# Performance work log

Measured on AMD Instinct MI355X. Metric: run time of the kernel, lower is better.

The kernel has to match this reference:

```python
import jax, jax.numpy as jnp
import numpy as np

EMBED_DIM = 1024
NUM_HEADS = 16
HEAD_DIM = EMBED_DIM // NUM_HEADS
BATCH = 4
SEQ = 2048


def setup_inputs() -> dict:
    key = jax.random.key(0)
    k1, k2, k3 = jax.random.split(key, 3)
    scale = 0.02
    x = jax.random.normal(k1, (BATCH, SEQ, EMBED_DIM), dtype=jnp.float32)
    Wqkv = jax.random.normal(k2, (EMBED_DIM, 3 * EMBED_DIM), dtype=jnp.float32) * scale
    bqkv = jnp.zeros((3 * EMBED_DIM,), dtype=jnp.float32)
    Wout = jax.random.normal(k3, (EMBED_DIM, EMBED_DIM), dtype=jnp.float32) * scale
    bout = jnp.zeros((EMBED_DIM,), dtype=jnp.float32)
    # causal mask: 1 where attention is allowed (lower triangle), 0 elsewhere
    mask = jnp.tril(jnp.ones((SEQ, SEQ), dtype=jnp.int32))
    return {"x": x, "mask": mask, "Wqkv": Wqkv, "bqkv": bqkv, "Wout": Wout, "bout": bout}


def reference(x, mask, Wqkv, bqkv, Wout, bout):
    B, S, E = x.shape
    H, D = NUM_HEADS, HEAD_DIM
    qkv = x @ Wqkv + bqkv                      # [B,S,3E]
    qkv = qkv.reshape(B, S, 3, H, D)
    qkv = jnp.transpose(qkv, (2, 0, 3, 1, 4))  # [3,B,H,S,D]
    Q, K, V = qkv[0], qkv[1], qkv[2]
    scores = jnp.einsum('bhqd,bhkd->bhqk', Q, K) / jnp.sqrt(jnp.float32(D))
    scores = jnp.where(mask[None, None] == 0, jnp.float32(-jnp.inf), scores)
    attn = jax.nn.softmax(scores, axis=-1)     # dropout omitted (eval mode)
    out = jnp.einsum('bhqk,bhkd->bhqd', attn, V)
    out = jnp.transpose(out, (0, 2, 1, 3)).reshape(B, S, E)
    return out @ Wout + bout
```

## Files before the change

### kernel.cpp

```cpp
#include <hip/hip_runtime.h>

#define S_LEN 2048
#define NH    16
#define HD    64
#define EMB   1024
#define NB    4
#define MROWS (NB * S_LEN)

typedef __attribute__((ext_vector_type(8))) short  short8;
typedef __attribute__((ext_vector_type(4))) float  float4_t;
typedef __attribute__((ext_vector_type(4))) int    int4_t;
union U8 { int4_t i; short8 s; };

__device__ __forceinline__ unsigned short f2bf(float f) {
    unsigned int x = __float_as_uint(f);
    unsigned int r = (x + 0x7fffu + ((x >> 16) & 1u)) >> 16;
    return (unsigned short)r;
}

__device__ __forceinline__ unsigned int cvtpk_bf16(float lo, float hi) {
    unsigned int r;
    asm("v_cvt_pk_bf16_f32 %0, %1, %2" : "=v"(r) : "v"(lo), "v"(hi));
    return r;
}

typedef const __attribute__((address_space(1))) unsigned int* gas_ptr;
typedef __attribute__((address_space(3))) unsigned int*       las_ptr;
__device__ __forceinline__ void gld_lds16(const void* g, void* l) {
    __builtin_amdgcn_global_load_lds((gas_ptr)g, (las_ptr)l, 16, 0, 0);
}

template<bool B> struct BoolC { static constexpr bool v = B; };

#define QSCALE 0.18033688011112042f

__global__ void cvt_f32_bf16(const float* __restrict__ in,
                             unsigned short* __restrict__ out, int n2) {
    int i = blockIdx.x * blockDim.x + threadIdx.x;
    if (i < n2) {
        float2 v = ((const float2*)in)[i];
        ushort2 o; o.x = f2bf(v.x); o.y = f2bf(v.y);
        ((ushort2*)out)[i] = o;
    }
}

__global__ void transpose_f32_bf16(const float* __restrict__ in,
                                   unsigned short* __restrict__ out, int R, int C) {
    __shared__ float tile[32][33];
    int n0 = blockIdx.x * 32, r0 = blockIdx.y * 32;
    int tx = threadIdx.x, ty = threadIdx.y;
#pragma unroll
    for (int i = 0; i < 4; ++i)
        tile[ty + i * 8][tx] = in[(size_t)(r0 + ty + i * 8) * C + n0 + tx];
    __syncthreads();
#pragma unroll
    for (int i = 0; i < 4; ++i)
        out[(size_t)(n0 + ty + i * 8) * R + r0 + tx] = f2bf(tile[tx][ty + i * 8]);
}

__global__ __launch_bounds__(256) void gemm_qkv(
    const unsigned short* __restrict__ X,
    const unsigned short* __restrict__ WT,
    const float* __restrict__ bias,
    unsigned short* __restrict__ Qb,
    unsigned short* __restrict__ Kb,
    unsigned short* __restrict__ VTb)
{
    __shared__ alignas(16) unsigned short As[128 * 32];
    __shared__ alignas(16) unsigned short Bs[128 * 32];
    const int K = 1024;
    int t = threadIdx.x;
    int wave = t >> 6, lane = t & 63, quad = lane >> 4, l = lane & 15;
    int bm = blockIdx.x * 128, bn = blockIdx.y * 128;
    int wm = (wave >> 1) * 64, wn = (wave & 1) * 64;

    float4_t z = {0.f, 0.f, 0.f, 0.f};
    float4_t acc[4][4];
#pragma unroll
    for (int i = 0; i < 4; ++i)
#pragma unroll
        for (int j = 0; j < 4; ++j) acc[i][j] = z;

    for (int kt = 0; kt < K / 32; ++kt) {
        int k0 = kt * 32;
        if (kt) __syncthreads();
#pragma unroll
        for (int it = 0; it < 2; ++it) {
            int c = t + 256 * it;
            int row = c >> 2, col = (c & 3) * 8;
            gld_lds16(&X [(size_t)(bm + row) * K + k0 + col], &As[c * 8]);
            gld_lds16(&WT[(size_t)(bn + row) * K + k0 + col], &Bs[c * 8]);
        }
        __syncthreads();
        short8 af[4], bfr[4];
#pragma unroll
        for (int i = 0; i < 4; ++i)
            af[i] = *(const short8*)&As[(wm + i * 16 + l) * 32 + quad * 8];
#pragma unroll
        for (int j = 0; j < 4; ++j)
            bfr[j] = *(const short8*)&Bs[(wn + j * 16 + l) * 32 + quad * 8];
#pragma unroll
        for (int i = 0; i < 4; ++i)
#pragma unroll
            for (int j = 0; j < 4; ++j)
                acc[i][j] = __builtin_amdgcn_mfma_f32_16x16x32_bf16(
                    af[i], bfr[j], acc[i][j], 0, 0, 0);
    }
#pragma unroll
    for (int j = 0; j < 4; ++j) {
        int gc = bn + wn + j * 16 + l;
        float bv = bias[gc];
        int which = gc >> 10, rem = gc & 1023;
        int h = rem >> 6, d = rem & 63;
        if (which == 2) {
            int bb = bm >> 11;
            size_t rowbase = ((size_t)(bb * NH + h) * HD + d) * S_LEN;
#pragma unroll
            for (int i = 0; i < 4; ++i) {
                unsigned int u0 = __float_as_uint(acc[i][j][0] + bv) + 0x8000u;
                unsigned int u1 = __float_as_uint(acc[i][j][1] + bv) + 0x8000u;
                unsigned int u2 = __float_as_uint(acc[i][j][2] + bv) + 0x8000u;
                unsigned int u3 = __float_as_uint(acc[i][j][3] + bv) + 0x8000u;
                uint2 vv;
                vv.x = __builtin_amdgcn_perm(u1, u0, 0x07060302u);
                vv.y = __builtin_amdgcn_perm(u3, u2, 0x07060302u);
                int s0 = (bm + wm + i * 16 + quad * 4) & 2047;
                int k6 = s0 & 63;
                int s0p = (s0 & ~63) | (((k6 >> 2) & 3) << 4) | (((k6 >> 4) & 3) << 2);
                *(uint2*)&VTb[rowbase + s0p] = vv;
            }
        } else {
#pragma unroll
            for (int i = 0; i < 4; ++i)
#pragma unroll
                for (int r = 0; r < 4; ++r) {
                    int gr = bm + wm + i * 16 + quad * 4 + r;
                    int b = gr >> 11, s = gr & 2047;
                    float ov = acc[i][j][r] + bv;
                    size_t bh2 = (size_t)(b * NH + h);
                    if (which == 0) Qb[(bh2 * S_LEN + s) * HD + d] = f2bf(ov * QSCALE);
                    else            Kb[(bh2 * S_LEN + s) * HD + d] = f2bf(ov);
                }
        }
    }
}

__global__ __launch_bounds__(256, 2) void flash_attn(
    const unsigned short* __restrict__ Qb,
    const unsigned short* __restrict__ Kb,
    const unsigned short* __restrict__ VTb,
    unsigned short* __restrict__ AO)
{
    __shared__ alignas(16) unsigned short smem[24576];

    int t = threadIdx.x, wave = t >> 6, lane = t & 63, quad = lane >> 4, cl = lane & 15;
    int blk = blockIdx.x;
    int bh = (blk & 7) + 8 * ((blk >> 3) & 7);
    int g = blk >> 6;
    int b = bh >> 4, h = bh & 15;
    int ci = (wave & 2) ? (62 - 2 * g + (wave & 1)) : (2 * g + (wave & 1));
    int qb = 32 * ci;
    int nkt = (ci >> 1) + 1;
    int nkt_max = 32 - g;

    const unsigned short* Qbase = Qb  + (size_t)bh * S_LEN * HD;
    const unsigned short* Kbase = Kb  + (size_t)bh * S_LEN * HD;
    const unsigned short* Vbase = VTb + (size_t)bh * HD * S_LEN;

    float4_t z = {0.f, 0.f, 0.f, 0.f};
    short8 onesf;
#pragma unroll
    for (int i = 0; i < 8; ++i) onesf[i] = (short)0x3F80;

    short8 bQ[2][2];
#pragma unroll
    for (int qt = 0; qt < 2; ++qt)
#pragma unroll
        for (int hh = 0; hh < 2; ++hh)
            bQ[qt][hh] = *(const short8*)&Qbase[(size_t)(qb + qt * 16 + cl) * HD + hh * 32 + quad * 8];

    float4_t acc[2][4], accs[2];
#pragma unroll
    for (int qt = 0; qt < 2; ++qt) {
        accs[qt] = z;
#pragma unroll
        for (int nb = 0; nb < 4; ++nb) acc[qt][nb] = z;
    }

    int koff0[4], koff1[4];
#pragma unroll
    for (int t4 = 0; t4 < 4; ++t4) {
        int row = t4 * 16 + cl, sw = row & 7;
        koff0[t4] = (row << 7) | ((quad ^ sw) << 4);
        koff1[t4] = (row << 7) | (((quad + 4) ^ sw) << 4);
    }
    int voffB[2][4];
#pragma unroll
    for (int p = 0; p < 2; ++p)
#pragma unroll
        for (int nb = 0; nb < 4; ++nb) {
            int row = nb * 16 + cl;
            voffB[p][nb] = 8192 + ((row << 7) | (((quad * 2 + p) ^ (row & 7)) << 4));
        }

    auto stage = [&](int kt, int slot) {
        int key0 = kt << 6;
        unsigned short* Kd = smem + slot * 8192;
        unsigned short* Vd = Kd + 4096;
#pragma unroll
        for (int i = 0; i < 2; ++i) {
            int s = t + 256 * i;
            int row = s >> 3, c16 = (s & 7) ^ (row & 7);
            gld_lds16(&Kbase[(size_t)(key0 + row) * HD + c16 * 8], &Kd[s * 8]);
            gld_lds16(&Vbase[(size_t)row * S_LEN + key0 + c16 * 8], &Vd[s * 8]);
        }
    };

    auto compute = [&](auto DIAGC, int slot, int key0) {
        constexpr bool DIAG = decltype(DIAGC)::v;
        const char* Kc = (const char*)(smem + slot * 8192);
        short8 aK0[4], aK1[4];
#pragma unroll
        for (int t4 = 0; t4 < 4; ++t4) {
            aK0[t4] = *(const short8*)(Kc + koff0[t4]);
            aK1[t4] = *(const short8*)(Kc + koff1[t4]);
        }
        U8 bv[2][4];
#pragma unroll
        for (int p = 0; p < 2; ++p)
#pragma unroll
            for (int nb = 0; nb < 4; ++nb)
                bv[p][nb].i = *(const int4_t*)(Kc + voffB[p][nb]);

#pragma unroll
        for (int qt = 0; qt < 2; ++qt) {
            unsigned int pk[4][2];
#pragma unroll
            for (int t4 = 0; t4 < 4; ++t4) {
                float4_t st = __builtin_amdgcn_mfma_f32_16x16x32_bf16(
                    aK1[t4], bQ[qt][1],
                    __builtin_amdgcn_mfma_f32_16x16x32_bf16(aK0[t4], bQ[qt][0], z, 0, 0, 0),
                    0, 0, 0);
                float e[4];
#pragma unroll
                for (int r = 0; r < 4; ++r) {
                    e[r] = __builtin_amdgcn_exp2f(st[r]);
                    if (DIAG) {
                        int key = key0 + t4 * 16 + quad * 4 + r;
                        e[r] = (key <= qb + qt * 16 + cl) ? e[r] : 0.f;
                    }
                }
                pk[t4][0] = cvtpk_bf16(e[0], e[1]);
                pk[t4][1] = cvtpk_bf16(e[2], e[3]);
            }
#pragma unroll
            for (int p = 0; p < 2; ++p) {
                U8 a; a.i = (int4_t){(int)pk[2 * p][0], (int)pk[2 * p][1],
                                     (int)pk[2 * p + 1][0], (int)pk[2 * p + 1][1]};
                accs[qt] = __builtin_amdgcn_mfma_f32_16x16x32_bf16(
                    a.s, onesf, accs[qt], 0, 0, 0);
#pragma unroll
                for (int nb = 0; nb < 4; ++nb)
                    acc[qt][nb] = __builtin_amdgcn_mfma_f32_16x16x32_bf16(
                        a.s, bv[p][nb].s, acc[qt][nb], 0, 0, 0);
            }
        }
    };

    stage(0, 0);
    if (nkt_max > 1) stage(1, 1);
    int cb = 0, sb = 2;
    for (int u = 0; u < nkt_max; ++u) {
        if (u + 1 < nkt_max) {
            asm volatile("s_waitcnt vmcnt(4)" ::: "memory");
        } else {
            asm volatile("s_waitcnt vmcnt(0)" ::: "memory");
        }
        __builtin_amdgcn_s_barrier();
        __builtin_amdgcn_sched_barrier(0);
        if (u + 2 < nkt_max) stage(u + 2, sb);
        if (u < nkt) {
            if (u == nkt - 1) compute(BoolC<true>{},  cb, u << 6);
            else              compute(BoolC<false>{}, cb, u << 6);
        }
        cb = (cb == 2) ? 0 : cb + 1;
        sb = (sb == 2) ? 0 : sb + 1;
    }

    __syncthreads();
    unsigned short* stgw = smem + wave * 1088;

#pragma unroll
    for (int qt = 0; qt < 2; ++qt) {
        float fr[4];
#pragma unroll
        for (int r = 0; r < 4; ++r) fr[r] = 1.f / accs[qt][r];
#pragma unroll
        for (int nb = 0; nb < 4; ++nb)
#pragma unroll
            for (int r = 0; r < 4; ++r) {
                unsigned int uu = __float_as_uint(acc[qt][nb][r] * fr[r]) + 0x8000u;
                stgw[(quad * 4 + r) * 68 + nb * 16 + cl] = (unsigned short)(uu >> 16);
            }
#pragma unroll
        for (int pass = 0; pass < 4; ++pass) {
            int idx = pass * 64 + lane;
            int row = idx >> 4, part = idx & 15;
            ushort4 v = *(const ushort4*)&stgw[row * 68 + part * 4];
            *(ushort4*)&AO[((size_t)b * S_LEN + qb + qt * 16 + row) * EMB + h * HD + part * 4] = v;
        }
    }
}

__global__ __launch_bounds__(256) void gemm_out(
    const unsigned short* __restrict__ A,
    const unsigned short* __restrict__ WT,
    const float* __restrict__ bias,
    float* __restrict__ out)
{
    __shared__ alignas(16) unsigned short As[128 * 32];
    __shared__ alignas(16) unsigned short Bs[128 * 32];
    const int K = 1024;
    int t = threadIdx.x;
    int wave = t >> 6, lane = t & 63, quad = lane >> 4, l = lane & 15;
    int bm = blockIdx.x * 128, bn = blockIdx.y * 128;
    int wm = (wave >> 1) * 64, wn = (wave & 1) * 64;

    float4_t z = {0.f, 0.f, 0.f, 0.f};
    float4_t acc[4][4];
#pragma unroll
    for (int i = 0; i < 4; ++i)
#pragma unroll
        for (int j = 0; j < 4; ++j) acc[i][j] = z;

    for (int kt = 0; kt < K / 32; ++kt) {
        int k0 = kt * 32;
        if (kt) __syncthreads();
#pragma unroll
        for (int it = 0; it < 2; ++it) {
            int c = t + 256 * it;
            int row = c >> 2, col = (c & 3) * 8;
            gld_lds16(&A [(size_t)(bm + row) * K + k0 + col], &As[c * 8]);
            gld_lds16(&WT[(size_t)(bn + row) * K + k0 + col], &Bs[c * 8]);
        }
        __syncthreads();
        short8 af[4], bfr[4];
#pragma unroll
        for (int i = 0; i < 4; ++i)
            af[i] = *(const short8*)&As[(wm + i * 16 + l) * 32 + quad * 8];
#pragma unroll
        for (int j = 0; j < 4; ++j)
            bfr[j] = *(const short8*)&Bs[(wn + j * 16 + l) * 32 + quad * 8];
#pragma unroll
        for (int i = 0; i < 4; ++i)
#pragma unroll
            for (int j = 0; j < 4; ++j)
                acc[i][j] = __builtin_amdgcn_mfma_f32_16x16x32_bf16(
                    af[i], bfr[j], acc[i][j], 0, 0, 0);
    }
#pragma unroll
    for (int j = 0; j < 4; ++j) {
        int gc = bn + wn + j * 16 + l;
        float bv = bias[gc];
#pragma unroll
        for (int i = 0; i < 4; ++i) {
#pragma unroll
            for (int r = 0; r < 4; ++r) {
                int gr = bm + wm + i * 16 + quad * 4 + r;
                out[(size_t)gr * EMB + gc] = acc[i][j][r] + bv;
            }
        }
    }
}

extern "C" void kernel_launch(void* const* d_in, const int* in_sizes, int n_in,
                              void* d_out, int out_size, void* d_ws, size_t ws_size,
                              hipStream_t stream) {
    const float* x    = (const float*)d_in[0];
    const float* Wqkv = (const float*)d_in[2];
    const float* bqkv = (const float*)d_in[3];
    const float* Wout = (const float*)d_in[4];
    const float* bout = (const float*)d_in[5];
    float* out = (float*)d_out;

    char* ws = (char*)d_ws;
    const size_t SZ = (size_t)NB * NH * S_LEN * HD * 2;
    unsigned short* Qb    = (unsigned short*)(ws);
    unsigned short* Kb    = (unsigned short*)(ws + SZ);
    unsigned short* VTb   = (unsigned short*)(ws + 2 * SZ);
    unsigned short* Xb    = (unsigned short*)(ws + 3 * SZ);
    unsigned short* AO    = (unsigned short*)(ws + 3 * SZ);
    unsigned short* WqkvT = (unsigned short*)(ws + 4 * SZ);
    unsigned short* WoutT = (unsigned short*)(ws + 4 * SZ + (size_t)3 * EMB * EMB * 2);

    int n2 = MROWS * EMB / 2;
    cvt_f32_bf16<<<dim3((n2 + 255) / 256), 256, 0, stream>>>(x, Xb, n2);
    dim3 tb(32, 8);
    transpose_f32_bf16<<<dim3(3 * EMB / 32, EMB / 32), tb, 0, stream>>>(Wqkv, WqkvT, EMB, 3 * EMB);
    transpose_f32_bf16<<<dim3(EMB / 32, EMB / 32), tb, 0, stream>>>(Wout, WoutT, EMB, EMB);
    gemm_qkv<<<dim3(MROWS / 128, 3 * EMB / 128), 256, 0, stream>>>(Xb, WqkvT, bqkv, Qb, Kb, VTb);
    flash_attn<<<dim3(1024), 256, 0, stream>>>(Qb, Kb, VTb, AO);
    gemm_out<<<dim3(MROWS / 128, EMB / 128), 256, 0, stream>>>(AO, WoutT, bout, out);
}
```

Measured before the change: 248.4 us.

## Triple-buffer LDS with async prefetch and XOR swizzle in projection GEMMs

```diff
diff --git a/kernel.cpp b/kernel.cpp
--- a/kernel.cpp
+++ b/kernel.cpp
@@ -58,7 +58,7 @@
         out[(size_t)(n0 + ty + i * 8) * R + r0 + tx] = f2bf(tile[tx][ty + i * 8]);
 }
 
-__global__ __launch_bounds__(256) void gemm_qkv(
+__global__ __launch_bounds__(256, 2) void gemm_qkv(
     const unsigned short* __restrict__ X,
     const unsigned short* __restrict__ WT,
     const float* __restrict__ bias,
@@ -66,13 +66,15 @@
     unsigned short* __restrict__ Kb,
     unsigned short* __restrict__ VTb)
 {
-    __shared__ alignas(16) unsigned short As[128 * 32];
-    __shared__ alignas(16) unsigned short Bs[128 * 32];
+    __shared__ alignas(16) unsigned short smemA[3 * 4096];
+    __shared__ alignas(16) unsigned short smemB[3 * 4096];
     const int K = 1024;
+    const int NT = K / 32;
     int t = threadIdx.x;
     int wave = t >> 6, lane = t & 63, quad = lane >> 4, l = lane & 15;
     int bm = blockIdx.x * 128, bn = blockIdx.y * 128;
     int wm = (wave >> 1) * 64, wn = (wave & 1) * 64;
+    int colrd = (quad ^ (l & 3)) * 8;
 
     float4_t z = {0.f, 0.f, 0.f, 0.f};
     float4_t acc[4][4];
@@ -81,31 +83,54 @@
 #pragma unroll
         for (int j = 0; j < 4; ++j) acc[i][j] = z;
 
-    for (int kt = 0; kt < K / 32; ++kt) {
+    auto stage = [&](int kt, int slot) {
         int k0 = kt * 32;
-        if (kt) __syncthreads();
+        unsigned short* Ad = smemA + slot * 4096;
+        unsigned short* Bd = smemB + slot * 4096;
 #pragma unroll
         for (int it = 0; it < 2; ++it) {
             int c = t + 256 * it;
-            int row = c >> 2, col = (c & 3) * 8;
-            gld_lds16(&X [(size_t)(bm + row) * K + k0 + col], &As[c * 8]);
-            gld_lds16(&WT[(size_t)(bn + row) * K + k0 + col], &Bs[c * 8]);
-        }
-        __syncthreads();
+            int row = c >> 2, col = ((c & 3) ^ (row & 3)) * 8;
+            gld_lds16(&X [(size_t)(bm + row) * K + k0 + col], &Ad[c * 8]);
+            gld_lds16(&WT[(size_t)(bn + row) * K + k0 + col], &Bd[c * 8]);
+        }
+    };
+
+    auto compute = [&](int slot) {
+        const unsigned short* Ac = smemA + slot * 4096;
+        const unsigned short* Bc = smemB + slot * 4096;
         short8 af[4], bfr[4];
 #pragma unroll
         for (int i = 0; i < 4; ++i)
-            af[i] = *(const short8*)&As[(wm + i * 16 + l) * 32 + quad * 8];
+            af[i] = *(const short8*)&Ac[(wm + i * 16 + l) * 32 + colrd];
 #pragma unroll
         for (int j = 0; j < 4; ++j)
-            bfr[j] = *(const short8*)&Bs[(wn + j * 16 + l) * 32 + quad * 8];
+            bfr[j] = *(const short8*)&Bc[(wn + j * 16 + l) * 32 + colrd];
 #pragma unroll
         for (int i = 0; i < 4; ++i)
 #pragma unroll
             for (int j = 0; j < 4; ++j)
                 acc[i][j] = __builtin_amdgcn_mfma_f32_16x16x32_bf16(
                     af[i], bfr[j], acc[i][j], 0, 0, 0);
-    }
+    };
+
+    stage(0, 0);
+    stage(1, 1);
+    int cs = 0, ss = 2;
+    for (int u = 0; u < NT; ++u) {
+        if (u + 1 < NT) {
+            asm volatile("s_waitcnt vmcnt(4)" ::: "memory");
+        } else {
+            asm volatile("s_waitcnt vmcnt(0)" ::: "memory");
+        }
+        __builtin_amdgcn_s_barrier();
+        __builtin_amdgcn_sched_barrier(0);
+        if (u + 2 < NT) stage(u + 2, ss);
+        compute(cs);
+        cs = (cs == 2) ? 0 : cs + 1;
+        ss = (ss == 2) ? 0 : ss + 1;
+    }
+
 #pragma unroll
     for (int j = 0; j < 4; ++j) {
         int gc = bn + wn + j * 16 + l;
@@ -117,13 +142,9 @@
             size_t rowbase = ((size_t)(bb * NH + h) * HD + d) * S_LEN;
 #pragma unroll
             for (int i = 0; i < 4; ++i) {
-                unsigned int u0 = __float_as_uint(acc[i][j][0] + bv) + 0x8000u;
-                unsigned int u1 = __float_as_uint(acc[i][j][1] + bv) + 0x8000u;
-                unsigned int u2 = __float_as_uint(acc[i][j][2] + bv) + 0x8000u;
-                unsigned int u3 = __float_as_uint(acc[i][j][3] + bv) + 0x8000u;
                 uint2 vv;
-                vv.x = __builtin_amdgcn_perm(u1, u0, 0x07060302u);
-                vv.y = __builtin_amdgcn_perm(u3, u2, 0x07060302u);
+                vv.x = cvtpk_bf16(acc[i][j][0] + bv, acc[i][j][1] + bv);
+                vv.y = cvtpk_bf16(acc[i][j][2] + bv, acc[i][j][3] + bv);
                 int s0 = (bm + wm + i * 16 + quad * 4) & 2047;
                 int k6 = s0 & 63;
                 int s0p = (s0 & ~63) | (((k6 >> 2) & 3) << 4) | (((k6 >> 4) & 3) << 2);
@@ -312,19 +333,21 @@
     }
 }
 
-__global__ __launch_bounds__(256) void gemm_out(
+__global__ __launch_bounds__(256, 2) void gemm_out(
     const unsigned short* __restrict__ A,
     const unsigned short* __restrict__ WT,
     const float* __restrict__ bias,
     float* __restrict__ out)
 {
-    __shared__ alignas(16) unsigned short As[128 * 32];
-    __shared__ alignas(16) unsigned short Bs[128 * 32];
+    __shared__ alignas(16) unsigned short smemA[3 * 4096];
+    __shared__ alignas(16) unsigned short smemB[3 * 4096];
     const int K = 1024;
+    const int NT = K / 32;
     int t = threadIdx.x;
     int wave = t >> 6, lane = t & 63, quad = lane >> 4, l = lane & 15;
     int bm = blockIdx.x * 128, bn = blockIdx.y * 128;
     int wm = (wave >> 1) * 64, wn = (wave & 1) * 64;
+    int colrd = (quad ^ (l & 3)) * 8;
 
     float4_t z = {0.f, 0.f, 0.f, 0.f};
     float4_t acc[4][4];
@@ -333,31 +356,54 @@
 #pragma unroll
         for (int j = 0; j < 4; ++j) acc[i][j] = z;
 
-    for (int kt = 0; kt < K / 32; ++kt) {
+    auto stage = [&](int kt, int slot) {
         int k0 = kt * 32;
-        if (kt) __syncthreads();
+        unsigned short* Ad = smemA + slot * 4096;
+        unsigned short* Bd = smemB + slot * 4096;
 #pragma unroll
         for (int it = 0; it < 2; ++it) {
             int c = t + 256 * it;
-            int row = c >> 2, col = (c & 3) * 8;
-            gld_lds16(&A [(size_t)(bm + row) * K + k0 + col], &As[c * 8]);
-            gld_lds16(&WT[(size_t)(bn + row) * K + k0 + col], &Bs[c * 8]);
-        }
-        __syncthreads();
+            int row = c >> 2, col = ((c & 3) ^ (row & 3)) * 8;
+            gld_lds16(&A [(size_t)(bm + row) * K + k0 + col], &Ad[c * 8]);
+            gld_lds16(&WT[(size_t)(bn + row) * K + k0 + col], &Bd[c * 8]);
+        }
+    };
+
+    auto compute = [&](int slot) {
+        const unsigned short* Ac = smemA + slot * 4096;
+        const unsigned short* Bc = smemB + slot * 4096;
         short8 af[4], bfr[4];
 #pragma unroll
         for (int i = 0; i < 4; ++i)
-            af[i] = *(const short8*)&As[(wm + i * 16 + l) * 32 + quad * 8];
+            af[i] = *(const short8*)&Ac[(wm + i * 16 + l) * 32 + colrd];
 #pragma unroll
         for (int j = 0; j < 4; ++j)
-            bfr[j] = *(const short8*)&Bs[(wn + j * 16 + l) * 32 + quad * 8];
+            bfr[j] = *(const short8*)&Bc[(wn + j * 16 + l) * 32 + colrd];
 #pragma unroll
         for (int i = 0; i < 4; ++i)
 #pragma unroll
             for (int j = 0; j < 4; ++j)
                 acc[i][j] = __builtin_amdgcn_mfma_f32_16x16x32_bf16(
                     af[i], bfr[j], acc[i][j], 0, 0, 0);
-    }
+    };
+
+    stage(0, 0);
+    stage(1, 1);
+    int cs = 0, ss = 2;
+    for (int u = 0; u < NT; ++u) {
+        if (u + 1 < NT) {
+            asm volatile("s_waitcnt vmcnt(4)" ::: "memory");
+        } else {
+            asm volatile("s_waitcnt vmcnt(0)" ::: "memory");
+        }
+        __builtin_amdgcn_s_barrier();
+        __builtin_amdgcn_sched_barrier(0);
+        if (u + 2 < NT) stage(u + 2, ss);
+        compute(cs);
+        cs = (cs == 2) ? 0 : cs + 1;
+        ss = (ss == 2) ? 0 : ss + 1;
+    }
+
 #pragma unroll
     for (int j = 0; j < 4; ++j) {
         int gc = bn + wn + j * 16 + l;
```

Measured after the change: 254.6 us. 1.02x slower.
